# Optimization experiments

Hardware: AMD Instinct MI355X
Metric: run time of the kernel (lower is better)

## Reference

```python
import jax, jax.numpy as jnp
import numpy as np

DEPTH = 2
NQ = 4  # 4 qubits -> 16-amplitude statevector per (batch, channel)


def setup_inputs() -> dict:
    key = jax.random.key(0)
    k1, k2 = jax.random.split(key)
    inputs = jax.random.normal(k1, (128, 32, 32, 512), dtype=jnp.float32)  # NHWC
    quantum_weights = jax.random.uniform(k2, (512, DEPTH, NQ, 3), dtype=jnp.float32) * (2.0 * np.pi)
    return {"inputs": inputs, "quantum_weights": quantum_weights}


def _ry(theta):
    # RY(theta) = [[cos(t/2), -sin(t/2)], [sin(t/2), cos(t/2)]]; theta shape (B, m)
    c = jnp.cos(theta / 2)
    s = jnp.sin(theta / 2)
    g = jnp.stack([jnp.stack([c, -s], axis=-1), jnp.stack([s, c], axis=-1)], axis=-2)
    return g.astype(jnp.complex64)  # (B, m, 2, 2)


def _rot(phi, theta, omega):
    # PennyLane Rot(phi, theta, omega) = RZ(omega) @ RY(theta) @ RZ(phi); args shape (m,)
    c = jnp.cos(theta / 2).astype(jnp.complex64)
    s = jnp.sin(theta / 2).astype(jnp.complex64)
    ep = jnp.exp(-0.5j * (phi + omega).astype(jnp.complex64))  # e^{-i(phi+omega)/2}
    em = jnp.exp(0.5j * (phi - omega).astype(jnp.complex64))   # e^{ i(phi-omega)/2}
    g00 = ep * c
    g01 = -em * s
    g10 = jnp.conj(em) * s
    g11 = jnp.conj(ep) * c
    return jnp.stack([jnp.stack([g00, g01], axis=-1), jnp.stack([g10, g11], axis=-1)], axis=-2)  # (m,2,2)


def _apply_1q(state, gate, wire):
    # state: (B, m, 2,2,2,2); gate: (B, m, 2, 2); contract on qubit axis 2+wire
    s = jnp.moveaxis(state, 2 + wire, -1)
    s = jnp.einsum('bmij,bm...j->bm...i', gate, s)
    return jnp.moveaxis(s, -1, 2 + wire)


def _cnot(state, control, target):
    s = jnp.moveaxis(state, (2 + control, 2 + target), (-2, -1))
    s = jnp.stack([s[..., 0, :], s[..., 1, ::-1]], axis=-2)  # flip target where control=1
    return jnp.moveaxis(s, (-2, -1), (2 + control, 2 + target))


def reference(inputs, quantum_weights):
    B, n, _, m = inputs.shape
    x = jnp.transpose(inputs, (0, 3, 1, 2))                     # (B, m, n, n)
    pooled = x.reshape(B, m, 2, n // 2, 2, n // 2).mean(axis=(3, 5))  # (B, m, 2, 2)
    angles = jnp.tanh(pooled.reshape(B, m, 4)) * jnp.pi                # (B, m, 4)

    # |0000> statevector per (batch, channel)
    state = jnp.zeros((B, m, 2, 2, 2, 2), dtype=jnp.complex64).at[:, :, 0, 0, 0, 0].set(1.0)

    # angle embedding: RY(x_k * pi) on wire k
    for k in range(NQ):
        state = _apply_1q(state, _ry(angles[..., k]), k)

    for layer in range(DEPTH):
        w = quantum_weights[:, layer]  # (m, NQ, 3)
        for k in range(NQ):
            g = _rot(w[:, k, 0], w[:, k, 1], w[:, k, 2])  # (m, 2, 2) per-channel
            state = _apply_1q(state, jnp.broadcast_to(g[None], (B, m, 2, 2)), k)
        for i in range(NQ):
            for j in range(i + 1, NQ):
                state = _cnot(state, i, j)

    # expval PauliZ(0) = P(q0=0) - P(q0=1)
    p = state.real ** 2 + state.imag ** 2          # (B, m, 2, 2, 2, 2)
    z = (p[:, :, 0] - p[:, :, 1]).sum(axis=(2, 3, 4))  # (B, m)
    return z.astype(inputs.dtype)
```

## Files before the change

### kernel.cpp

```cpp
#include <hip/hip_runtime.h>
#include <math.h>


#define B_DIM   128
#define N_DIM   32
#define M_DIM   512
#define PI_F    3.14159265358979323846f

__global__ __launch_bounds__(256)
void pool_kernel(const float* __restrict__ in, float* __restrict__ ws) {
    int blk   = blockIdx.x;
    int chunk = blk & 3;
    int qi    = (blk >> 2) & 1;
    int b     = blk >> 3;
    int t     = threadIdx.x;
    int m4    = t & 127;
    int joff  = t >> 7;
    int i0    = qi * 16 + chunk * 4;

    const float4* in4 = (const float4*)in + (size_t)b * (N_DIM * N_DIM * (M_DIM / 4));

    float4 a0 = make_float4(0.f, 0.f, 0.f, 0.f);
    float4 a1 = make_float4(0.f, 0.f, 0.f, 0.f);

    for (int r = 0; r < 4; ++r) {
        int i = i0 + r;
        const float4* row = in4 + (size_t)i * (N_DIM * (M_DIM / 4));
        #pragma unroll
        for (int jp = 0; jp < 16; ++jp) {
            int j = jp * 2 + joff;
            float4 v = row[(j << 7) + m4];
            if (jp < 8) { a0.x += v.x; a0.y += v.y; a0.z += v.z; a0.w += v.w; }
            else        { a1.x += v.x; a1.y += v.y; a1.z += v.z; a1.w += v.w; }
        }
    }

    __shared__ float4 red[2][128];
    if (joff) { red[0][m4] = a0; red[1][m4] = a1; }
    __syncthreads();
    if (!joff) {
        float4 r0 = red[0][m4], r1 = red[1][m4];
        a0.x += r0.x; a0.y += r0.y; a0.z += r0.z; a0.w += r0.w;
        a1.x += r1.x; a1.y += r1.y; a1.z += r1.z; a1.w += r1.w;
        float4* w4 = (float4*)ws;
        size_t base = ((size_t)((b * 2 + qi) * 4 + chunk) * 2) * 128 + m4;
        w4[base]       = a0;
        w4[base + 128] = a1;
    }
}

struct Cpx { float x, y; };

template<int M>
__device__ __forceinline__ void apply1q(float* re, float* im,
                                        Cpx g00, Cpx g01, Cpx g10, Cpx g11) {
    #pragma unroll
    for (int s = 0; s < 16; ++s) {
        if (s & M) continue;
        int s1 = s | M;
        float ar = re[s],  ai = im[s];
        float br = re[s1], bi = im[s1];
        re[s]  = g00.x * ar - g00.y * ai + g01.x * br - g01.y * bi;
        im[s]  = g00.x * ai + g00.y * ar + g01.x * bi + g01.y * br;
        re[s1] = g10.x * ar - g10.y * ai + g11.x * br - g11.y * bi;
        im[s1] = g10.x * ai + g10.y * ar + g11.x * bi + g11.y * br;
    }
}

template<int MC, int MT>
__device__ __forceinline__ void cnot(float* re, float* im) {
    #pragma unroll
    for (int s = 0; s < 16; ++s) {
        if ((s & MC) && !(s & MT)) {
            int s1 = s | MT;
            float t;
            t = re[s]; re[s] = re[s1]; re[s1] = t;
            t = im[s]; im[s] = im[s1]; im[s1] = t;
        }
    }
}

__device__ __forceinline__ void rot_gate(float phi, float theta, float omega,
                                         Cpx& g00, Cpx& g01, Cpx& g10, Cpx& g11) {
    float st, ct, sa, ca, sd, cd;
    __sincosf(0.5f * theta, &st, &ct);
    __sincosf(0.5f * (phi + omega), &sa, &ca);
    __sincosf(0.5f * (phi - omega), &sd, &cd);
    g00.x =  ca * ct;  g00.y = -sa * ct;
    g01.x = -cd * st;  g01.y = -sd * st;
    g10.x =  cd * st;  g10.y = -sd * st;
    g11.x =  ca * ct;  g11.y =  sa * ct;
}

__global__ __launch_bounds__(256)
void quantum_kernel(const float* __restrict__ ws, const float* __restrict__ qw,
                    float* __restrict__ out) {
    int idx = blockIdx.x * 256 + threadIdx.x;
    int m = idx & (M_DIM - 1);
    int b = idx >> 9;

    float ang[4];
    #pragma unroll
    for (int qi = 0; qi < 2; ++qi) {
        #pragma unroll
        for (int qj = 0; qj < 2; ++qj) {
            float s = 0.f;
            #pragma unroll
            for (int c = 0; c < 4; ++c) {
                s += ws[((size_t)((b * 2 + qi) * 4 + c) * 2 + qj) * M_DIM + m];
            }
            ang[qi * 2 + qj] = tanhf(s * (1.0f / 256.0f)) * PI_F;
        }
    }

    float cs[4], sn[4];
    #pragma unroll
    for (int k = 0; k < 4; ++k) __sincosf(0.5f * ang[k], &sn[k], &cs[k]);

    float re[16], im[16];
    #pragma unroll
    for (int s = 0; s < 16; ++s) {
        re[s] = ((s & 8) ? sn[0] : cs[0]) * ((s & 4) ? sn[1] : cs[1]) *
                ((s & 2) ? sn[2] : cs[2]) * ((s & 1) ? sn[3] : cs[3]);
        im[s] = 0.f;
    }

    const float* wbase = qw + (size_t)m * 24;
    #pragma unroll
    for (int layer = 0; layer < 2; ++layer) {
        const float* wl = wbase + layer * 12;
        Cpx g00, g01, g10, g11;
        rot_gate(wl[0],  wl[1],  wl[2],  g00, g01, g10, g11); apply1q<8>(re, im, g00, g01, g10, g11);
        rot_gate(wl[3],  wl[4],  wl[5],  g00, g01, g10, g11); apply1q<4>(re, im, g00, g01, g10, g11);
        rot_gate(wl[6],  wl[7],  wl[8],  g00, g01, g10, g11); apply1q<2>(re, im, g00, g01, g10, g11);
        rot_gate(wl[9],  wl[10], wl[11], g00, g01, g10, g11); apply1q<1>(re, im, g00, g01, g10, g11);
        cnot<8, 4>(re, im);
        cnot<8, 2>(re, im);
        cnot<8, 1>(re, im);
        cnot<4, 2>(re, im);
        cnot<4, 1>(re, im);
        cnot<2, 1>(re, im);
    }

    float z = 0.f;
    #pragma unroll
    for (int s = 0; s < 16; ++s) {
        float p = re[s] * re[s] + im[s] * im[s];
        z += (s & 8) ? -p : p;
    }
    out[idx] = z;
}

extern "C" void kernel_launch(void* const* d_in, const int* in_sizes, int n_in,
                              void* d_out, int out_size, void* d_ws, size_t ws_size,
                              hipStream_t stream) {
    const float* in = (const float*)d_in[0];
    const float* qw = (const float*)d_in[1];
    float* out = (float*)d_out;
    float* ws  = (float*)d_ws;

    (void)in_sizes; (void)n_in; (void)out_size; (void)ws_size;

    pool_kernel<<<B_DIM * 2 * 4, 256, 0, stream>>>(in, ws);
    quantum_kernel<<<(B_DIM * M_DIM) / 256, 256, 0, stream>>>(ws, qw, out);
}
```

Before: 361.0 us.

## Fuse pooling and quantum circuit into a single kernel via LDS reduction

```diff
diff --git a/kernel.cpp b/kernel.cpp
--- a/kernel.cpp
+++ b/kernel.cpp
@@ -3,51 +3,8 @@
 
 
 #define B_DIM   128
-#define N_DIM   32
 #define M_DIM   512
 #define PI_F    3.14159265358979323846f
-
-__global__ __launch_bounds__(256)
-void pool_kernel(const float* __restrict__ in, float* __restrict__ ws) {
-    int blk   = blockIdx.x;
-    int chunk = blk & 3;
-    int qi    = (blk >> 2) & 1;
-    int b     = blk >> 3;
-    int t     = threadIdx.x;
-    int m4    = t & 127;
-    int joff  = t >> 7;
-    int i0    = qi * 16 + chunk * 4;
-
-    const float4* in4 = (const float4*)in + (size_t)b * (N_DIM * N_DIM * (M_DIM / 4));
-
-    float4 a0 = make_float4(0.f, 0.f, 0.f, 0.f);
-    float4 a1 = make_float4(0.f, 0.f, 0.f, 0.f);
-
-    for (int r = 0; r < 4; ++r) {
-        int i = i0 + r;
-        const float4* row = in4 + (size_t)i * (N_DIM * (M_DIM / 4));
-        #pragma unroll
-        for (int jp = 0; jp < 16; ++jp) {
-            int j = jp * 2 + joff;
-            float4 v = row[(j << 7) + m4];
-            if (jp < 8) { a0.x += v.x; a0.y += v.y; a0.z += v.z; a0.w += v.w; }
-            else        { a1.x += v.x; a1.y += v.y; a1.z += v.z; a1.w += v.w; }
-        }
-    }
-
-    __shared__ float4 red[2][128];
-    if (joff) { red[0][m4] = a0; red[1][m4] = a1; }
-    __syncthreads();
-    if (!joff) {
-        float4 r0 = red[0][m4], r1 = red[1][m4];
-        a0.x += r0.x; a0.y += r0.y; a0.z += r0.z; a0.w += r0.w;
-        a1.x += r1.x; a1.y += r1.y; a1.z += r1.z; a1.w += r1.w;
-        float4* w4 = (float4*)ws;
-        size_t base = ((size_t)((b * 2 + qi) * 4 + chunk) * 2) * 128 + m4;
-        w4[base]       = a0;
-        w4[base + 128] = a1;
-    }
-}
 
 struct Cpx { float x, y; };
 
@@ -93,62 +50,105 @@
 }
 
 __global__ __launch_bounds__(256)
-void quantum_kernel(const float* __restrict__ ws, const float* __restrict__ qw,
-                    float* __restrict__ out) {
-    int idx = blockIdx.x * 256 + threadIdx.x;
-    int m = idx & (M_DIM - 1);
-    int b = idx >> 9;
+void qpool_fused_kernel(const float* __restrict__ in, const float* __restrict__ qw,
+                        float* __restrict__ out) {
+    int blk = blockIdx.x;
+    int mt  = blk & 3;
+    int b   = blk >> 2;
+    int t   = threadIdx.x;
+    int mc  = t & 31;
+    int w   = t >> 5;
 
-    float ang[4];
+    const float4* in4 = (const float4*)in
+        + (size_t)b * (32 * 32 * (M_DIM / 4)) + mt * 32 + mc;
+
+    float4 acc[2][2];
+    #pragma unroll
+    for (int qi = 0; qi < 2; ++qi)
+        #pragma unroll
+        for (int qj = 0; qj < 2; ++qj)
+            acc[qi][qj] = make_float4(0.f, 0.f, 0.f, 0.f);
+
     #pragma unroll
     for (int qi = 0; qi < 2; ++qi) {
         #pragma unroll
-        for (int qj = 0; qj < 2; ++qj) {
-            float s = 0.f;
+        for (int rh = 0; rh < 2; ++rh) {
+            int i = qi * 16 + rh * 8 + w;
+            const float4* row = in4 + (size_t)i * (32 * (M_DIM / 4));
             #pragma unroll
-            for (int c = 0; c < 4; ++c) {
-                s += ws[((size_t)((b * 2 + qi) * 4 + c) * 2 + qj) * M_DIM + m];
+            for (int j = 0; j < 32; ++j) {
+                float4 v = row[j * (M_DIM / 4)];
+                int qj = j >> 4;
+                acc[qi][qj].x += v.x; acc[qi][qj].y += v.y;
+                acc[qi][qj].z += v.z; acc[qi][qj].w += v.w;
             }
-            ang[qi * 2 + qj] = tanhf(s * (1.0f / 256.0f)) * PI_F;
         }
     }
 
-    float cs[4], sn[4];
+    __shared__ float4 lds[8][2][2][32];
     #pragma unroll
-    for (int k = 0; k < 4; ++k) __sincosf(0.5f * ang[k], &sn[k], &cs[k]);
+    for (int qi = 0; qi < 2; ++qi)
+        #pragma unroll
+        for (int qj = 0; qj < 2; ++qj)
+            lds[w][qi][qj][mc] = acc[qi][qj];
+    __syncthreads();
 
-    float re[16], im[16];
-    #pragma unroll
-    for (int s = 0; s < 16; ++s) {
-        re[s] = ((s & 8) ? sn[0] : cs[0]) * ((s & 4) ? sn[1] : cs[1]) *
-                ((s & 2) ? sn[2] : cs[2]) * ((s & 1) ? sn[3] : cs[3]);
-        im[s] = 0.f;
+    if (t < 128) {
+        int c = t;
+        int m = mt * 128 + c;
+
+        float ang[4];
+        const float* ldsf = (const float*)lds;
+        #pragma unroll
+        for (int qi = 0; qi < 2; ++qi) {
+            #pragma unroll
+            for (int qj = 0; qj < 2; ++qj) {
+                float s = 0.f;
+                #pragma unroll
+                for (int ww = 0; ww < 8; ++ww) {
+                    s += ldsf[(((ww * 2 + qi) * 2 + qj) * 128) + c];
+                }
+                ang[qi * 2 + qj] = tanhf(s * (1.0f / 256.0f)) * PI_F;
+            }
+        }
+
+        float cs[4], sn[4];
+        #pragma unroll
+        for (int k = 0; k < 4; ++k) __sincosf(0.5f * ang[k], &sn[k], &cs[k]);
+
+        float re[16], im[16];
+        #pragma unroll
+        for (int s = 0; s < 16; ++s) {
+            re[s] = ((s & 8) ? sn[0] : cs[0]) * ((s & 4) ? sn[1] : cs[1]) *
+                    ((s & 2) ? sn[2] : cs[2]) * ((s & 1) ? sn[3] : cs[3]);
+            im[s] = 0.f;
+        }
+
+        const float* wbase = qw + (size_t)m * 24;
+        #pragma unroll
+        for (int layer = 0; layer < 2; ++layer) {
+            const float* wl = wbase + layer * 12;
+            Cpx g00, g01, g10, g11;
+            rot_gate(wl[0],  wl[1],  wl[2],  g00, g01, g10, g11); apply1q<8>(re, im, g00, g01, g10, g11);
+            rot_gate(wl[3],  wl[4],  wl[5],  g00, g01, g10, g11); apply1q<4>(re, im, g00, g01, g10, g11);
+            rot_gate(wl[6],  wl[7],  wl[8],  g00, g01, g10, g11); apply1q<2>(re, im, g00, g01, g10, g11);
+            rot_gate(wl[9],  wl[10], wl[11], g00, g01, g10, g11); apply1q<1>(re, im, g00, g01, g10, g11);
+            cnot<8, 4>(re, im);
+            cnot<8, 2>(re, im);
+            cnot<8, 1>(re, im);
+            cnot<4, 2>(re, im);
+            cnot<4, 1>(re, im);
+            cnot<2, 1>(re, im);
+        }
+
+        float z = 0.f;
+        #pragma unroll
+        for (int s = 0; s < 16; ++s) {
+            float p = re[s] * re[s] + im[s] * im[s];
+            z += (s & 8) ? -p : p;
+        }
+        out[(size_t)b * M_DIM + m] = z;
     }
-
-    const float* wbase = qw + (size_t)m * 24;
-    #pragma unroll
-    for (int layer = 0; layer < 2; ++layer) {
-        const float* wl = wbase + layer * 12;
-        Cpx g00, g01, g10, g11;
-        rot_gate(wl[0],  wl[1],  wl[2],  g00, g01, g10, g11); apply1q<8>(re, im, g00, g01, g10, g11);
-        rot_gate(wl[3],  wl[4],  wl[5],  g00, g01, g10, g11); apply1q<4>(re, im, g00, g01, g10, g11);
-        rot_gate(wl[6],  wl[7],  wl[8],  g00, g01, g10, g11); apply1q<2>(re, im, g00, g01, g10, g11);
-        rot_gate(wl[9],  wl[10], wl[11], g00, g01, g10, g11); apply1q<1>(re, im, g00, g01, g10, g11);
-        cnot<8, 4>(re, im);
-        cnot<8, 2>(re, im);
-        cnot<8, 1>(re, im);
-        cnot<4, 2>(re, im);
-        cnot<4, 1>(re, im);
-        cnot<2, 1>(re, im);
-    }
-
-    float z = 0.f;
-    #pragma unroll
-    for (int s = 0; s < 16; ++s) {
-        float p = re[s] * re[s] + im[s] * im[s];
-        z += (s & 8) ? -p : p;
-    }
-    out[idx] = z;
 }
 
 extern "C" void kernel_launch(void* const* d_in, const int* in_sizes, int n_in,
@@ -157,10 +157,8 @@
     const float* in = (const float*)d_in[0];
     const float* qw = (const float*)d_in[1];
     float* out = (float*)d_out;
-    float* ws  = (float*)d_ws;
 
-    (void)in_sizes; (void)n_in; (void)out_size; (void)ws_size;
+    (void)in_sizes; (void)n_in; (void)out_size; (void)d_ws; (void)ws_size;
 
-    pool_kernel<<<B_DIM * 2 * 4, 256, 0, stream>>>(in, ws);
-    quantum_kernel<<<(B_DIM * M_DIM) / 256, 256, 0, stream>>>(ws, qw, out);
+    qpool_fused_kernel<<<B_DIM * 4, 256, 0, stream>>>(in, qw, out);
 }
```

Measured after the change: 363.0 us. No clear change (+0.5%).
